# Kernel tuning notes

Hardware: AMD Instinct MI355X
Metric: run time of the kernel (lower is better)

Reference implementation:

```python
import jax, jax.numpy as jnp
import numpy as np

LATENT = 256; INPUT = 128; NUNITS = 256; DEC_OUT = 128
NTRAJ = 256; NTP = 512
INTERP = 2  # hard-coded in the original forward

def _mlp_sig(x, w1, b1, w2, b2):
    return jax.nn.sigmoid(jnp.tanh(x @ w1 + b1) @ w2 + b2)

def _mlp_lin(x, w1, b1, w2, b2):
    return jnp.tanh(x @ w1 + b1) @ w2 + b2

def _gru_step(y, yt, x, ug, ugt, rg, ns):
    # x: [N, 2*INPUT]; first half = features, second half = observation mask channels
    xh = x[:, :INPUT]
    yc = jnp.concatenate([y, xh], axis=-1)                 # [N, LATENT+INPUT]
    u = _mlp_sig(yc, *ug)
    ut = _mlp_sig(yc, *ugt)
    r = _mlp_sig(yc, *rg)
    new_state = _mlp_lin(jnp.concatenate([y * r, xh], axis=-1), *ns)
    new_y = (1.0 - u) * new_state + u * y
    new_yt = (1.0 - ut) * new_state + ut * yt
    mask = (jnp.sum(x[:, INPUT:], axis=-1, keepdims=True) > 0).astype(x.dtype)
    return mask * new_y + (1.0 - mask) * y, mask * new_yt + (1.0 - mask) * yt

def setup_inputs():
    key = jax.random.key(0)
    ks = iter(jax.random.split(key, 32))
    def p(shape):
        return jax.random.normal(next(ks), shape, dtype=jnp.float32) * 0.05
    d = {}
    d["data"] = jax.random.normal(next(ks), (NTRAJ, NTP, 2 * INPUT), dtype=jnp.float32)
    dts = jax.random.uniform(next(ks), (NTRAJ, NTP), dtype=jnp.float32) + 0.1
    d["time_steps"] = jnp.cumsum(dts, axis=1)              # strictly increasing times
    gin = LATENT + INPUT
    for name in ("ug", "ugt", "rg", "rgt", "ns"):
        d[name + "_w1"] = p((gin, NUNITS)); d[name + "_b1"] = jnp.zeros((NUNITS,), jnp.float32)
        d[name + "_w2"] = p((NUNITS, LATENT)); d[name + "_b2"] = jnp.zeros((LATENT,), jnp.float32)
    d["dk_w1"] = p((LATENT, LATENT)); d["dk_b1"] = jnp.zeros((LATENT,), jnp.float32)
    d["dk_w2"] = p((LATENT, 1)); d["dk_b2"] = jnp.zeros((1,), jnp.float32)
    d["dec_w"] = p((LATENT, DEC_OUT)); d["dec_b"] = jnp.zeros((DEC_OUT,), jnp.float32)
    return d

def reference(data, time_steps,
              ug_w1, ug_b1, ug_w2, ug_b2,
              ugt_w1, ugt_b1, ugt_w2, ugt_b2,
              rg_w1, rg_b1, rg_w2, rg_b2,
              rgt_w1, rgt_b1, rgt_w2, rgt_b2,
              ns_w1, ns_b1, ns_w2, ns_b2,
              dk_w1, dk_b1, dk_w2, dk_b2,
              dec_w, dec_b):
    # Note: reset_gate_target (rgt_*) is computed but never used in the original forward.
    ug = (ug_w1, ug_b1, ug_w2, ug_b2)
    ugt = (ugt_w1, ugt_b1, ugt_w2, ugt_b2)
    rg = (rg_w1, rg_b1, rg_w2, rg_b2)
    ns = (ns_w1, ns_b1, ns_w2, ns_b2)
    n_traj = data.shape[0]
    lin = jnp.linspace(0.0, 1.0, INTERP + 1, dtype=data.dtype)  # [3]
    y0 = jnp.zeros((n_traj, LATENT), data.dtype)
    # step i=0: no decay interpolation, yi_decay = prev_y (zeros)
    y, yt = _gru_step(y0, y0, data[:, 0, :], ug, ugt, rg, ns)
    dts = time_steps[:, 1:] - time_steps[:, :-1]                # [N, T-1]
    xs = jnp.moveaxis(data[:, 1:, :], 1, 0)                     # [T-1, N, 2I]

    def step(carry, inp):
        y, yt = carry
        x, dt = inp
        decay = jax.nn.relu(jax.nn.relu(y @ dk_w1 + dk_b1) @ dk_w2 + dk_b2)  # [N,1]
        e = jnp.exp(-decay * (dt[:, None] * lin[None, :]))                   # [N,3]
        ydec = yt[:, None, :] + (y - yt)[:, None, :] * e[:, :, None]         # [N,3,L]
        vol = jnp.mean(ydec[:, :-1, :] @ dec_w + dec_b, axis=-2)             # [N,D]
        y2, yt2 = _gru_step(ydec[:, -1, :], yt, x, ug, ugt, rg, ns)
        return (y2, yt2), vol

    (y, yt), vols = jax.lax.scan(step, (y, yt), (xs, dts.T))
    prev_y = y[None, :, :]                       # [1, N, L]
    volume_dt = jnp.transpose(vols, (1, 0, 2))   # [N, T-1, D]
    return prev_y, volume_dt, dts
```

## Files before the change

### kernel.cpp

```cpp
#include <hip/hip_runtime.h>
#include <hip/hip_fp16.h>

#define NTRAJ   256
#define NTP     512
#define NSTEPS  511
#define LATENT  256
#define INPUT   128
#define DEC_OUT 128

#define OUT_VOL ((size_t)NTRAJ * LATENT)
#define OUT_DTS (OUT_VOL + (size_t)NTRAJ * NSTEPS * DEC_OUT)

#define WU_UG1  0
#define WU_UG2  49152
#define WU_UGT1 81920
#define WU_UGT2 131072
#define WU_RG1  163840
#define WU_RG2  212992
#define WU_NS1  245760
#define WU_NS2  294912
#define WU_DK1  327680
#define WU_DEC  360448
#define WU_TOT  376832

typedef _Float16 h2_t __attribute__((ext_vector_type(2)));
union U32H2 { unsigned int u; h2_t h; };

__device__ __forceinline__ float dot2f(unsigned int wu, unsigned int xu, float acc) {
#if defined(__has_builtin) && __has_builtin(__builtin_amdgcn_fdot2)
    U32H2 a, b; a.u = wu; b.u = xu;
    return __builtin_amdgcn_fdot2(a.h, b.h, acc, false);
#else
    U32H2 a, b; a.u = wu; b.u = xu;
    return acc + (float)a.h.x * (float)b.h.x + (float)a.h.y * (float)b.h.y;
#endif
}

__device__ __forceinline__ float wred(float v) {
    #pragma unroll
    for (int off = 32; off; off >>= 1) v += __shfl_down(v, off, 64);
    return v;
}
__device__ __forceinline__ float fast_sigmoid(float x) { return 1.0f / (1.0f + __expf(-x)); }
__device__ __forceinline__ float fast_tanh(float x) {
    float e = __expf(2.0f * x);
    return 1.0f - 2.0f / (e + 1.0f);
}
__device__ __forceinline__ unsigned int packpair(float v) {
    float vn = __shfl_xor(v, 1, 64);
    U32H2 r; r.h.x = (_Float16)v; r.h.y = (_Float16)vn;
    return r.u;
}
__device__ __forceinline__ unsigned int pk2(float a, float b) {
    U32H2 r; r.h.x = (_Float16)a; r.h.y = (_Float16)b; return r.u;
}
__device__ __forceinline__ float4 bfly4(float4 v, int m) {
    v.x += __shfl_xor(v.x, m, 64);
    v.y += __shfl_xor(v.y, m, 64);
    v.z += __shfl_xor(v.z, m, 64);
    v.w += __shfl_xor(v.w, m, 64);
    return v;
}

extern "C" __global__ void __launch_bounds__(256)
convert_w(const float* __restrict__ ug_w1, const float* __restrict__ ug_w2,
          const float* __restrict__ ugt_w1, const float* __restrict__ ugt_w2,
          const float* __restrict__ rg_w1, const float* __restrict__ rg_w2,
          const float* __restrict__ ns_w1, const float* __restrict__ ns_w2,
          const float* __restrict__ dk_w1, const float* __restrict__ dec_w,
          unsigned int* __restrict__ ws)
{
    const int i = blockIdx.x * 256 + threadIdx.x;
    const float* s; int o; int cbits;
    if      (i < WU_UG2)  { s = ug_w1;  o = i;           cbits = 8; }
    else if (i < WU_UGT1) { s = ug_w2;  o = i - WU_UG2;  cbits = 8; }
    else if (i < WU_UGT2) { s = ugt_w1; o = i - WU_UGT1; cbits = 8; }
    else if (i < WU_RG1)  { s = ugt_w2; o = i - WU_UGT2; cbits = 8; }
    else if (i < WU_RG2)  { s = rg_w1;  o = i - WU_RG1;  cbits = 8; }
    else if (i < WU_NS1)  { s = rg_w2;  o = i - WU_RG2;  cbits = 8; }
    else if (i < WU_NS2)  { s = ns_w1;  o = i - WU_NS1;  cbits = 8; }
    else if (i < WU_DK1)  { s = ns_w2;  o = i - WU_NS2;  cbits = 8; }
    else if (i < WU_DEC)  { s = dk_w1;  o = i - WU_DK1;  cbits = 8; }
    else                  { s = dec_w;  o = i - WU_DEC;  cbits = 7; }
    const int C  = 1 << cbits;
    const int kp = o >> cbits;
    const int c  = o & (C - 1);
    const float v0 = s[(2 * kp) * C + c];
    const float v1 = s[(2 * kp + 1) * C + c];
    const unsigned int h0 = __half_as_ushort(__float2half(v0));
    const unsigned int h1 = __half_as_ushort(__float2half(v1));
    ws[i] = h0 | (h1 << 16);
}

#define DOT1(acc, wv, xv) { \
    acc.x = dot2f((wv).x, (xv), acc.x); acc.y = dot2f((wv).y, (xv), acc.y); \
    acc.z = dot2f((wv).z, (xv), acc.z); acc.w = dot2f((wv).w, (xv), acc.w); }

extern "C" __global__ void __launch_bounds__(512, 2)
rnn_decay_kernel4(const float* __restrict__ data, const float* __restrict__ ts,
                  const float* __restrict__ ug_b1, const float* __restrict__ ug_b2,
                  const float* __restrict__ ugt_b1, const float* __restrict__ ugt_b2,
                  const float* __restrict__ rg_b1, const float* __restrict__ rg_b2,
                  const float* __restrict__ ns_b1, const float* __restrict__ ns_b2,
                  const float* __restrict__ dk_b1, const float* __restrict__ dk_w2,
                  const float* __restrict__ dk_b2, const float* __restrict__ dec_b,
                  const unsigned int* __restrict__ wsu, float* __restrict__ out)
{
    __shared__ __align__(16) unsigned int s_in_h[192];
    __shared__ __align__(16) unsigned int s_ns_h[192];
    __shared__ __align__(16) unsigned int s_y_h[128];
    __shared__ __align__(16) unsigned int s_a_h[128];
    __shared__ __align__(16) unsigned int s_b_h[128];
    __shared__ __align__(16) unsigned int s_c_h[128];
    __shared__ __align__(16) unsigned int s_v_h[128];
    __shared__ float s_red[12];

    const int tid  = threadIdx.x;
    const int w    = tid >> 6;
    const int lane = tid & 63;
    const int c    = tid & 255;
    const int sl   = lane >> 3;
    const int g    = lane & 7;
    const int c0   = (w << 5) + (g << 2);
    const int h2b  = c0 >> 1;
    const int sld  = lane >> 2;
    const int c0d  = (w << 4) + ((lane & 3) << 2);
    const int traj = blockIdx.x;

    const unsigned int* UG1  = wsu + WU_UG1;  const unsigned int* UG2  = wsu + WU_UG2;
    const unsigned int* UGT1 = wsu + WU_UGT1; const unsigned int* UGT2 = wsu + WU_UGT2;
    const unsigned int* RG1  = wsu + WU_RG1;  const unsigned int* RG2  = wsu + WU_RG2;
    const unsigned int* NS1  = wsu + WU_NS1;  const unsigned int* NS2  = wsu + WU_NS2;
    const unsigned int* DK1  = wsu + WU_DK1;  const unsigned int* DECW = wsu + WU_DEC;

    const float* dbase = data + (size_t)traj * NTP * (2 * INPUT);
    const float* tbase = ts + (size_t)traj * NTP;
    float* vol_out = out + OUT_VOL + (size_t)traj * NSTEPS * DEC_OUT;
    float* dts_out = out + OUT_DTS + (size_t)traj * NSTEPS;

    if (tid < 256)
        for (int t0 = c; t0 < NSTEPS; t0 += 256)
            dts_out[t0] = tbase[t0 + 1] - tbase[t0];

    const float4 ugb1v  = *(const float4*)(ug_b1  + c0);
    const float4 ugtb1v = *(const float4*)(ugt_b1 + c0);
    const float4 rgb1v  = *(const float4*)(rg_b1  + c0);
    const float4 nsb1v  = *(const float4*)(ns_b1  + c0);
    const float4 ugb2v  = *(const float4*)(ug_b2  + c0);
    const float4 ugtb2v = *(const float4*)(ugt_b2 + c0);
    const float4 rgb2v  = *(const float4*)(rg_b2  + c0);
    const float4 nsb2v  = *(const float4*)(ns_b2  + c0);
    const float4 dkb1v  = *(const float4*)(dk_b1  + c0);
    const float4 dkw2v  = *(const float4*)(dk_w2  + c0);
    const float4 decbv  = *(const float4*)(dec_b  + c0d);
    const float  dkb2s  = dk_b2[0];

    float4 y4  = make_float4(0.f, 0.f, 0.f, 0.f);
    float4 yt4 = y4;

    for (int t = -1; t < NSTEPS; ++t) {
        const bool first = (t < 0);

        float dt_t = 0.f;
        if (!first) dt_t = tbase[t + 1] - tbase[t];
        float xval = 0.f;
        if (tid < 256)
            xval = first ? dbase[c] : dbase[(size_t)(t + 1) * 256 + c];

        if (!first) {
            float4 aD = make_float4(0.f, 0.f, 0.f, 0.f);
            #pragma unroll 4
            for (int i = 0; i < 16; ++i) {
                const int kp = sl + (i << 3);
                const unsigned int xv = s_y_h[kp];
                const uint4 wv = *(const uint4*)(DK1 + (size_t)kp * 256 + c0);
                DOT1(aD, wv, xv);
            }
            aD = bfly4(aD, 8); aD = bfly4(aD, 16); aD = bfly4(aD, 32);
            float sdk = fmaxf(aD.x + dkb1v.x, 0.f) * dkw2v.x
                      + fmaxf(aD.y + dkb1v.y, 0.f) * dkw2v.y
                      + fmaxf(aD.z + dkb1v.z, 0.f) * dkw2v.z
                      + fmaxf(aD.w + dkb1v.w, 0.f) * dkw2v.w;
            sdk += __shfl_xor(sdk, 1, 64);
            sdk += __shfl_xor(sdk, 2, 64);
            sdk += __shfl_xor(sdk, 4, 64);
            if (lane == 0) s_red[4 + w] = sdk;
        }
        if (tid < 256) {
            float mv = (c >= 128) ? xval : 0.f;
            mv = wred(mv);
            if (lane == 0) s_red[w] = mv;
            if (c < 128) {
                const unsigned int px = packpair(xval);
                if (!(lane & 1)) { s_in_h[128 + (c >> 1)] = px; s_ns_h[128 + (c >> 1)] = px; }
            }
            if (first && !(lane & 1)) s_in_h[c >> 1] = 0u;
        }
        __syncthreads();

        const bool maskv = (s_red[0] + s_red[1] + s_red[2] + s_red[3]) > 0.f;
        float4 ydec4 = make_float4(0.f, 0.f, 0.f, 0.f);
        if (!first) {
            const float decay = fmaxf(s_red[4] + s_red[5] + s_red[6] + s_red[7]
                                    + s_red[8] + s_red[9] + s_red[10] + s_red[11]
                                    + dkb2s, 0.f);
            const float ef = __expf(-decay * dt_t);
            const float eh = __expf(-0.5f * decay * dt_t);
            float4 vol4;
            ydec4.x = yt4.x + (y4.x - yt4.x) * ef;
            ydec4.y = yt4.y + (y4.y - yt4.y) * ef;
            ydec4.z = yt4.z + (y4.z - yt4.z) * ef;
            ydec4.w = yt4.w + (y4.w - yt4.w) * ef;
            vol4.x = 0.5f * (y4.x + yt4.x + (y4.x - yt4.x) * eh);
            vol4.y = 0.5f * (y4.y + yt4.y + (y4.y - yt4.y) * eh);
            vol4.z = 0.5f * (y4.z + yt4.z + (y4.z - yt4.z) * eh);
            vol4.w = 0.5f * (y4.w + yt4.w + (y4.w - yt4.w) * eh);
            if (!sl) {
                uint2 pd; pd.x = pk2(ydec4.x, ydec4.y); pd.y = pk2(ydec4.z, ydec4.w);
                uint2 pv; pv.x = pk2(vol4.x, vol4.y);   pv.y = pk2(vol4.z, vol4.w);
                *(uint2*)(s_in_h + h2b) = pd;
                *(uint2*)(s_v_h + h2b)  = pv;
            }
        }
        __syncthreads();

        if (!first) {
            float4 aE = make_float4(0.f, 0.f, 0.f, 0.f);
            #pragma unroll 4
            for (int i = 0; i < 8; ++i) {
                const int kp = sld + (i << 4);
                const unsigned int xv = s_v_h[kp];
                const uint4 wv = *(const uint4*)(DECW + (size_t)kp * 128 + c0d);
                DOT1(aE, wv, xv);
            }
            aE = bfly4(aE, 4); aE = bfly4(aE, 8); aE = bfly4(aE, 16); aE = bfly4(aE, 32);
            if (sld == 0) {
                float4 o;
                o.x = aE.x + decbv.x; o.y = aE.y + decbv.y;
                o.z = aE.z + decbv.z; o.w = aE.w + decbv.w;
                *(float4*)(vol_out + (size_t)t * DEC_OUT + c0d) = o;
            }
        }
        {
            float4 aA = make_float4(0.f, 0.f, 0.f, 0.f), aB = aA, aC = aA;
            #pragma unroll 4
            for (int i = 0; i < 24; ++i) {
                const int kp = sl + (i << 3);
                const unsigned int xv = s_in_h[kp];
                const uint4 wa = *(const uint4*)(UG1  + (size_t)kp * 256 + c0);
                const uint4 wb = *(const uint4*)(UGT1 + (size_t)kp * 256 + c0);
                const uint4 wc = *(const uint4*)(RG1  + (size_t)kp * 256 + c0);
                DOT1(aA, wa, xv); DOT1(aB, wb, xv); DOT1(aC, wc, xv);
            }
            aA = bfly4(aA, 8); aA = bfly4(aA, 16); aA = bfly4(aA, 32);
            aB = bfly4(aB, 8); aB = bfly4(aB, 16); aB = bfly4(aB, 32);
            aC = bfly4(aC, 8); aC = bfly4(aC, 16); aC = bfly4(aC, 32);
            if (!sl) {
                uint2 pa, pb, pc;
                pa.x = pk2(fast_tanh(aA.x + ugb1v.x),  fast_tanh(aA.y + ugb1v.y));
                pa.y = pk2(fast_tanh(aA.z + ugb1v.z),  fast_tanh(aA.w + ugb1v.w));
                pb.x = pk2(fast_tanh(aB.x + ugtb1v.x), fast_tanh(aB.y + ugtb1v.y));
                pb.y = pk2(fast_tanh(aB.z + ugtb1v.z), fast_tanh(aB.w + ugtb1v.w));
                pc.x = pk2(fast_tanh(aC.x + rgb1v.x),  fast_tanh(aC.y + rgb1v.y));
                pc.y = pk2(fast_tanh(aC.z + rgb1v.z),  fast_tanh(aC.w + rgb1v.w));
                *(uint2*)(s_a_h + h2b) = pa;
                *(uint2*)(s_b_h + h2b) = pb;
                *(uint2*)(s_c_h + h2b) = pc;
            }
        }
        __syncthreads();

        float4 u4, ut4;
        {
            float4 aA = make_float4(0.f, 0.f, 0.f, 0.f), aB = aA, aC = aA;
            #pragma unroll 4
            for (int i = 0; i < 16; ++i) {
                const int kp = sl + (i << 3);
                const unsigned int xa = s_a_h[kp];
                const unsigned int xb = s_b_h[kp];
                const unsigned int xc = s_c_h[kp];
                const uint4 wa = *(const uint4*)(UG2  + (size_t)kp * 256 + c0);
                const uint4 wb = *(const uint4*)(UGT2 + (size_t)kp * 256 + c0);
                const uint4 wc = *(const uint4*)(RG2  + (size_t)kp * 256 + c0);
                DOT1(aA, wa, xa); DOT1(aB, wb, xb); DOT1(aC, wc, xc);
            }
            aA = bfly4(aA, 8); aA = bfly4(aA, 16); aA = bfly4(aA, 32);
            aB = bfly4(aB, 8); aB = bfly4(aB, 16); aB = bfly4(aB, 32);
            aC = bfly4(aC, 8); aC = bfly4(aC, 16); aC = bfly4(aC, 32);
            u4.x  = fast_sigmoid(aA.x + ugb2v.x);  u4.y  = fast_sigmoid(aA.y + ugb2v.y);
            u4.z  = fast_sigmoid(aA.z + ugb2v.z);  u4.w  = fast_sigmoid(aA.w + ugb2v.w);
            ut4.x = fast_sigmoid(aB.x + ugtb2v.x); ut4.y = fast_sigmoid(aB.y + ugtb2v.y);
            ut4.z = fast_sigmoid(aB.z + ugtb2v.z); ut4.w = fast_sigmoid(aB.w + ugtb2v.w);
            const float rx = fast_sigmoid(aC.x + rgb2v.x);
            const float ry = fast_sigmoid(aC.y + rgb2v.y);
            const float rz = fast_sigmoid(aC.z + rgb2v.z);
            const float rw = fast_sigmoid(aC.w + rgb2v.w);
            if (!sl) {
                uint2 pn;
                pn.x = pk2(ydec4.x * rx, ydec4.y * ry);
                pn.y = pk2(ydec4.z * rz, ydec4.w * rw);
                *(uint2*)(s_ns_h + h2b) = pn;
            }
        }
        __syncthreads();

        {
            float4 aA = make_float4(0.f, 0.f, 0.f, 0.f);
            #pragma unroll 4
            for (int i = 0; i < 24; ++i) {
                const int kp = sl + (i << 3);
                const unsigned int xv = s_ns_h[kp];
                const uint4 wa = *(const uint4*)(NS1 + (size_t)kp * 256 + c0);
                DOT1(aA, wa, xv);
            }
            aA = bfly4(aA, 8); aA = bfly4(aA, 16); aA = bfly4(aA, 32);
            if (!sl) {
                uint2 ph;
                ph.x = pk2(fast_tanh(aA.x + nsb1v.x), fast_tanh(aA.y + nsb1v.y));
                ph.y = pk2(fast_tanh(aA.z + nsb1v.z), fast_tanh(aA.w + nsb1v.w));
                *(uint2*)(s_a_h + h2b) = ph;
            }
        }
        __syncthreads();

        {
            float4 aA = make_float4(0.f, 0.f, 0.f, 0.f);
            #pragma unroll 4
            for (int i = 0; i < 16; ++i) {
                const int kp = sl + (i << 3);
                const unsigned int xv = s_a_h[kp];
                const uint4 wa = *(const uint4*)(NS2 + (size_t)kp * 256 + c0);
                DOT1(aA, wa, xv);
            }
            aA = bfly4(aA, 8); aA = bfly4(aA, 16); aA = bfly4(aA, 32);
            const float nx = aA.x + nsb2v.x, ny_ = aA.y + nsb2v.y;
            const float nz = aA.z + nsb2v.z, nw = aA.w + nsb2v.w;
            const float yx = (1.f - u4.x) * nx  + u4.x * ydec4.x;
            const float yy = (1.f - u4.y) * ny_ + u4.y * ydec4.y;
            const float yz = (1.f - u4.z) * nz  + u4.z * ydec4.z;
            const float yw = (1.f - u4.w) * nw  + u4.w * ydec4.w;
            const float tx = (1.f - ut4.x) * nx  + ut4.x * yt4.x;
            const float ty = (1.f - ut4.y) * ny_ + ut4.y * yt4.y;
            const float tz = (1.f - ut4.z) * nz  + ut4.z * yt4.z;
            const float tw = (1.f - ut4.w) * nw  + ut4.w * yt4.w;
            y4.x  = maskv ? yx : ydec4.x;  y4.y  = maskv ? yy : ydec4.y;
            y4.z  = maskv ? yz : ydec4.z;  y4.w  = maskv ? yw : ydec4.w;
            yt4.x = maskv ? tx : yt4.x;    yt4.y = maskv ? ty : yt4.y;
            yt4.z = maskv ? tz : yt4.z;    yt4.w = maskv ? tw : yt4.w;
            if (!sl) {
                uint2 py;
                py.x = pk2(y4.x, y4.y); py.y = pk2(y4.z, y4.w);
                *(uint2*)(s_y_h + h2b) = py;
            }
        }
        __syncthreads();
    }

    if (!sl)
        *(float4*)(out + (size_t)traj * 256 + c0) = y4;
}

extern "C" void kernel_launch(void* const* d_in, const int* in_sizes, int n_in,
                              void* d_out, int out_size, void* d_ws, size_t ws_size,
                              hipStream_t stream) {
    const float* data   = (const float*)d_in[0];
    const float* ts     = (const float*)d_in[1];
    const float* ug_w1  = (const float*)d_in[2];
    const float* ug_b1  = (const float*)d_in[3];
    const float* ug_w2  = (const float*)d_in[4];
    const float* ug_b2  = (const float*)d_in[5];
    const float* ugt_w1 = (const float*)d_in[6];
    const float* ugt_b1 = (const float*)d_in[7];
    const float* ugt_w2 = (const float*)d_in[8];
    const float* ugt_b2 = (const float*)d_in[9];
    const float* rg_w1  = (const float*)d_in[10];
    const float* rg_b1  = (const float*)d_in[11];
    const float* rg_w2  = (const float*)d_in[12];
    const float* rg_b2  = (const float*)d_in[13];
    const float* ns_w1  = (const float*)d_in[18];
    const float* ns_b1  = (const float*)d_in[19];
    const float* ns_w2  = (const float*)d_in[20];
    const float* ns_b2  = (const float*)d_in[21];
    const float* dk_w1  = (const float*)d_in[22];
    const float* dk_b1  = (const float*)d_in[23];
    const float* dk_w2  = (const float*)d_in[24];
    const float* dk_b2  = (const float*)d_in[25];
    const float* dec_w  = (const float*)d_in[26];
    const float* dec_b  = (const float*)d_in[27];

    unsigned int* wsu = (unsigned int*)d_ws;

    convert_w<<<WU_TOT / 256, 256, 0, stream>>>(ug_w1, ug_w2, ugt_w1, ugt_w2,
                                                rg_w1, rg_w2, ns_w1, ns_w2,
                                                dk_w1, dec_w, wsu);

    rnn_decay_kernel4<<<NTRAJ, 512, 0, stream>>>(
        data, ts, ug_b1, ug_b2, ugt_b1, ugt_b2, rg_b1, rg_b2, ns_b1, ns_b2,
        dk_b1, dk_w2, dk_b2, dec_b, wsu, (float*)d_out);
}
```

Before: 8.042 ms.

## Double threads per block to 1024 and halve per-wave columns in GRU kernel

Launches the per-trajectory recurrent kernel with 1024 threads instead of 512. Each of the 16 waves now owns 16 output columns instead of 32, and the reduction dimension is split across 16 lane slices instead of 8. This adds one extra butterfly stage per matvec and widens the decay partial-sum reduction to 16 wave entries. Bias vectors are now loaded inside the time loop rather than held in registers, to cut register pressure enough to fit 1024 threads. The aim is to shorten each serial timestep's latency with more parallel lanes, at the cost of extra shuffles and repeated cached bias loads.

Measured after the change: 10.13 ms. +25.9%, slower.

```diff
diff --git a/kernel.cpp b/kernel.cpp
--- a/kernel.cpp
+++ b/kernel.cpp
@@ -96,8 +96,8 @@
     acc.x = dot2f((wv).x, (xv), acc.x); acc.y = dot2f((wv).y, (xv), acc.y); \
     acc.z = dot2f((wv).z, (xv), acc.z); acc.w = dot2f((wv).w, (xv), acc.w); }
 
-extern "C" __global__ void __launch_bounds__(512, 2)
-rnn_decay_kernel4(const float* __restrict__ data, const float* __restrict__ ts,
+extern "C" __global__ void __launch_bounds__(1024, 4)
+rnn_decay_kernel6(const float* __restrict__ data, const float* __restrict__ ts,
                   const float* __restrict__ ug_b1, const float* __restrict__ ug_b2,
                   const float* __restrict__ ugt_b1, const float* __restrict__ ugt_b2,
                   const float* __restrict__ rg_b1, const float* __restrict__ rg_b2,
@@ -113,18 +113,18 @@
     __shared__ __align__(16) unsigned int s_b_h[128];
     __shared__ __align__(16) unsigned int s_c_h[128];
     __shared__ __align__(16) unsigned int s_v_h[128];
-    __shared__ float s_red[12];
+    __shared__ __align__(16) float s_red[20];
 
     const int tid  = threadIdx.x;
     const int w    = tid >> 6;
     const int lane = tid & 63;
     const int c    = tid & 255;
-    const int sl   = lane >> 3;
-    const int g    = lane & 7;
-    const int c0   = (w << 5) + (g << 2);
+    const int sl   = lane >> 2;
+    const int g    = lane & 3;
+    const int c0   = (w << 4) + (g << 2);
     const int h2b  = c0 >> 1;
-    const int sld  = lane >> 2;
-    const int c0d  = (w << 4) + ((lane & 3) << 2);
+    const int sld  = lane >> 1;
+    const int c0d  = (w << 3) + ((lane & 1) << 2);
     const int traj = blockIdx.x;
 
     const unsigned int* UG1  = wsu + WU_UG1;  const unsigned int* UG2  = wsu + WU_UG2;
@@ -142,18 +142,7 @@
         for (int t0 = c; t0 < NSTEPS; t0 += 256)
             dts_out[t0] = tbase[t0 + 1] - tbase[t0];
 
-    const float4 ugb1v  = *(const float4*)(ug_b1  + c0);
-    const float4 ugtb1v = *(const float4*)(ugt_b1 + c0);
-    const float4 rgb1v  = *(const float4*)(rg_b1  + c0);
-    const float4 nsb1v  = *(const float4*)(ns_b1  + c0);
-    const float4 ugb2v  = *(const float4*)(ug_b2  + c0);
-    const float4 ugtb2v = *(const float4*)(ugt_b2 + c0);
-    const float4 rgb2v  = *(const float4*)(rg_b2  + c0);
-    const float4 nsb2v  = *(const float4*)(ns_b2  + c0);
-    const float4 dkb1v  = *(const float4*)(dk_b1  + c0);
-    const float4 dkw2v  = *(const float4*)(dk_w2  + c0);
-    const float4 decbv  = *(const float4*)(dec_b  + c0d);
-    const float  dkb2s  = dk_b2[0];
+    const float dkb2s = dk_b2[0];
 
     float4 y4  = make_float4(0.f, 0.f, 0.f, 0.f);
     float4 yt4 = y4;
@@ -170,20 +159,21 @@
         if (!first) {
             float4 aD = make_float4(0.f, 0.f, 0.f, 0.f);
             #pragma unroll 4
-            for (int i = 0; i < 16; ++i) {
-                const int kp = sl + (i << 3);
+            for (int i = 0; i < 8; ++i) {
+                const int kp = sl + (i << 4);
                 const unsigned int xv = s_y_h[kp];
                 const uint4 wv = *(const uint4*)(DK1 + (size_t)kp * 256 + c0);
                 DOT1(aD, wv, xv);
             }
-            aD = bfly4(aD, 8); aD = bfly4(aD, 16); aD = bfly4(aD, 32);
+            aD = bfly4(aD, 4); aD = bfly4(aD, 8); aD = bfly4(aD, 16); aD = bfly4(aD, 32);
+            const float4 dkb1v = *(const float4*)(dk_b1 + c0);
+            const float4 dkw2v = *(const float4*)(dk_w2 + c0);
             float sdk = fmaxf(aD.x + dkb1v.x, 0.f) * dkw2v.x
                       + fmaxf(aD.y + dkb1v.y, 0.f) * dkw2v.y
                       + fmaxf(aD.z + dkb1v.z, 0.f) * dkw2v.z
                       + fmaxf(aD.w + dkb1v.w, 0.f) * dkw2v.w;
             sdk += __shfl_xor(sdk, 1, 64);
             sdk += __shfl_xor(sdk, 2, 64);
-            sdk += __shfl_xor(sdk, 4, 64);
             if (lane == 0) s_red[4 + w] = sdk;
         }
         if (tid < 256) {
@@ -201,9 +191,10 @@
         const bool maskv = (s_red[0] + s_red[1] + s_red[2] + s_red[3]) > 0.f;
         float4 ydec4 = make_float4(0.f, 0.f, 0.f, 0.f);
         if (!first) {
-            const float decay = fmaxf(s_red[4] + s_red[5] + s_red[6] + s_red[7]
-                                    + s_red[8] + s_red[9] + s_red[10] + s_red[11]
-                                    + dkb2s, 0.f);
+            float dsum = dkb2s;
+            #pragma unroll
+            for (int i = 0; i < 16; ++i) dsum += s_red[4 + i];
+            const float decay = fmaxf(dsum, 0.f);
             const float ef = __expf(-decay * dt_t);
             const float eh = __expf(-0.5f * decay * dt_t);
             float4 vol4;
@@ -226,15 +217,17 @@
 
         if (!first) {
             float4 aE = make_float4(0.f, 0.f, 0.f, 0.f);
-            #pragma unroll 4
-            for (int i = 0; i < 8; ++i) {
-                const int kp = sld + (i << 4);
+            #pragma unroll
+            for (int i = 0; i < 4; ++i) {
+                const int kp = sld + (i << 5);
                 const unsigned int xv = s_v_h[kp];
                 const uint4 wv = *(const uint4*)(DECW + (size_t)kp * 128 + c0d);
                 DOT1(aE, wv, xv);
             }
-            aE = bfly4(aE, 4); aE = bfly4(aE, 8); aE = bfly4(aE, 16); aE = bfly4(aE, 32);
+            aE = bfly4(aE, 2); aE = bfly4(aE, 4); aE = bfly4(aE, 8);
+            aE = bfly4(aE, 16); aE = bfly4(aE, 32);
             if (sld == 0) {
+                const float4 decbv = *(const float4*)(dec_b + c0d);
                 float4 o;
                 o.x = aE.x + decbv.x; o.y = aE.y + decbv.y;
                 o.z = aE.z + decbv.z; o.w = aE.w + decbv.w;
@@ -244,18 +237,21 @@
         {
             float4 aA = make_float4(0.f, 0.f, 0.f, 0.f), aB = aA, aC = aA;
             #pragma unroll 4
-            for (int i = 0; i < 24; ++i) {
-                const int kp = sl + (i << 3);
+            for (int i = 0; i < 12; ++i) {
+                const int kp = sl + (i << 4);
                 const unsigned int xv = s_in_h[kp];
                 const uint4 wa = *(const uint4*)(UG1  + (size_t)kp * 256 + c0);
                 const uint4 wb = *(const uint4*)(UGT1 + (size_t)kp * 256 + c0);
                 const uint4 wc = *(const uint4*)(RG1  + (size_t)kp * 256 + c0);
                 DOT1(aA, wa, xv); DOT1(aB, wb, xv); DOT1(aC, wc, xv);
             }
-            aA = bfly4(aA, 8); aA = bfly4(aA, 16); aA = bfly4(aA, 32);
-            aB = bfly4(aB, 8); aB = bfly4(aB, 16); aB = bfly4(aB, 32);
-            aC = bfly4(aC, 8); aC = bfly4(aC, 16); aC = bfly4(aC, 32);
+            aA = bfly4(aA, 4); aA = bfly4(aA, 8); aA = bfly4(aA, 16); aA = bfly4(aA, 32);
+            aB = bfly4(aB, 4); aB = bfly4(aB, 8); aB = bfly4(aB, 16); aB = bfly4(aB, 32);
+            aC = bfly4(aC, 4); aC = bfly4(aC, 8); aC = bfly4(aC, 16); aC = bfly4(aC, 32);
             if (!sl) {
+                const float4 ugb1v  = *(const float4*)(ug_b1  + c0);
+                const float4 ugtb1v = *(const float4*)(ugt_b1 + c0);
+                const float4 rgb1v  = *(const float4*)(rg_b1  + c0);
                 uint2 pa, pb, pc;
                 pa.x = pk2(fast_tanh(aA.x + ugb1v.x),  fast_tanh(aA.y + ugb1v.y));
                 pa.y = pk2(fast_tanh(aA.z + ugb1v.z),  fast_tanh(aA.w + ugb1v.w));
@@ -274,8 +270,8 @@
         {
             float4 aA = make_float4(0.f, 0.f, 0.f, 0.f), aB = aA, aC = aA;
             #pragma unroll 4
-            for (int i = 0; i < 16; ++i) {
-                const int kp = sl + (i << 3);
+            for (int i = 0; i < 8; ++i) {
+                const int kp = sl + (i << 4);
                 const unsigned int xa = s_a_h[kp];
                 const unsigned int xb = s_b_h[kp];
                 const unsigned int xc = s_c_h[kp];
@@ -284,9 +280,12 @@
                 const uint4 wc = *(const uint4*)(RG2  + (size_t)kp * 256 + c0);
                 DOT1(aA, wa, xa); DOT1(aB, wb, xb); DOT1(aC, wc, xc);
             }
-            aA = bfly4(aA, 8); aA = bfly4(aA, 16); aA = bfly4(aA, 32);
-            aB = bfly4(aB, 8); aB = bfly4(aB, 16); aB = bfly4(aB, 32);
-            aC = bfly4(aC, 8); aC = bfly4(aC, 16); aC = bfly4(aC, 32);
+            aA = bfly4(aA, 4); aA = bfly4(aA, 8); aA = bfly4(aA, 16); aA = bfly4(aA, 32);
+            aB = bfly4(aB, 4); aB = bfly4(aB, 8); aB = bfly4(aB, 16); aB = bfly4(aB, 32);
+            aC = bfly4(aC, 4); aC = bfly4(aC, 8); aC = bfly4(aC, 16); aC = bfly4(aC, 32);
+            const float4 ugb2v  = *(const float4*)(ug_b2  + c0);
+            const float4 ugtb2v = *(const float4*)(ugt_b2 + c0);
+            const float4 rgb2v  = *(const float4*)(rg_b2  + c0);
             u4.x  = fast_sigmoid(aA.x + ugb2v.x);  u4.y  = fast_sigmoid(aA.y + ugb2v.y);
             u4.z  = fast_sigmoid(aA.z + ugb2v.z);  u4.w  = fast_sigmoid(aA.w + ugb2v.w);
             ut4.x = fast_sigmoid(aB.x + ugtb2v.x); ut4.y = fast_sigmoid(aB.y + ugtb2v.y);
@@ -307,14 +306,15 @@
         {
             float4 aA = make_float4(0.f, 0.f, 0.f, 0.f);
             #pragma unroll 4
-            for (int i = 0; i < 24; ++i) {
-                const int kp = sl + (i << 3);
+            for (int i = 0; i < 12; ++i) {
+                const int kp = sl + (i << 4);
                 const unsigned int xv = s_ns_h[kp];
                 const uint4 wa = *(const uint4*)(NS1 + (size_t)kp * 256 + c0);
                 DOT1(aA, wa, xv);
             }
-            aA = bfly4(aA, 8); aA = bfly4(aA, 16); aA = bfly4(aA, 32);
+            aA = bfly4(aA, 4); aA = bfly4(aA, 8); aA = bfly4(aA, 16); aA = bfly4(aA, 32);
             if (!sl) {
+                const float4 nsb1v = *(const float4*)(ns_b1 + c0);
                 uint2 ph;
                 ph.x = pk2(fast_tanh(aA.x + nsb1v.x), fast_tanh(aA.y + nsb1v.y));
                 ph.y = pk2(fast_tanh(aA.z + nsb1v.z), fast_tanh(aA.w + nsb1v.w));
@@ -326,13 +326,14 @@
         {
             float4 aA = make_float4(0.f, 0.f, 0.f, 0.f);
             #pragma unroll 4
-            for (int i = 0; i < 16; ++i) {
-                const int kp = sl + (i << 3);
+            for (int i = 0; i < 8; ++i) {
+                const int kp = sl + (i << 4);
                 const unsigned int xv = s_a_h[kp];
                 const uint4 wa = *(const uint4*)(NS2 + (size_t)kp * 256 + c0);
                 DOT1(aA, wa, xv);
             }
-            aA = bfly4(aA, 8); aA = bfly4(aA, 16); aA = bfly4(aA, 32);
+            aA = bfly4(aA, 4); aA = bfly4(aA, 8); aA = bfly4(aA, 16); aA = bfly4(aA, 32);
+            const float4 nsb2v = *(const float4*)(ns_b2 + c0);
             const float nx = aA.x + nsb2v.x, ny_ = aA.y + nsb2v.y;
             const float nz = aA.z + nsb2v.z, nw = aA.w + nsb2v.w;
             const float yx = (1.f - u4.x) * nx  + u4.x * ydec4.x;
@@ -394,7 +395,7 @@
                                                 rg_w1, rg_w2, ns_w1, ns_w2,
                                                 dk_w1, dec_w, wsu);
 
-    rnn_decay_kernel4<<<NTRAJ, 512, 0, stream>>>(
+    rnn_decay_kernel6<<<NTRAJ, 1024, 0, stream>>>(
         data, ts, ug_b1, ug_b2, ugt_b1, ugt_b2, rg_b1, rg_b2, ns_b1, ns_b2,
         dk_b1, dk_w2, dk_b2, dec_b, wsu, (float*)d_out);
 }
```
